# Performance work log

Hardware: AMD Instinct MI355X
Metric: run time of the kernel (lower is better)

Reference implementation:

```python
import jax, jax.numpy as jnp
import numpy as np

G, NP, C, H, L = 64, 512, 128, 4, 4
N = G * NP            # 32768 nodes
E = N * 16            # 524288 edges
HD = C // H
BN_EPS = 1e-5


def _bn(x, g, b):
    # BatchNorm1d, training-mode (biased batch statistics over nodes)
    m = x.mean(axis=0)
    v = jnp.var(x, axis=0)
    return (x - m) * jax.lax.rsqrt(v + BN_EPS) * g + b


def setup_inputs() -> dict:
    key = jax.random.key(0)
    ks = iter(jax.random.split(key, 64))
    rn = lambda shape, s=0.05: jax.random.normal(next(ks), shape, jnp.float32) * s
    inp = {}
    inp["x"] = jax.random.normal(next(ks), (N, 32), jnp.float32)
    inp["edge_attr"] = jax.random.normal(next(ks), (E, 16), jnp.float32)
    epg = E // G  # edges per graph; endpoints stay within each graph
    off = jnp.repeat(jnp.arange(G), epg) * NP
    src = jax.random.randint(next(ks), (E,), 0, NP) + off
    dst = jax.random.randint(next(ks), (E,), 0, NP) + off
    inp["edge_index"] = jnp.stack([src, dst]).astype(jnp.int32)
    inp["batch"] = jnp.repeat(jnp.arange(G), NP).astype(jnp.int32)
    inp["np_w"] = rn((32, C)); inp["np_b"] = jnp.zeros((C,), jnp.float32)
    inp["ep_w"] = rn((16, C)); inp["ep_b"] = jnp.zeros((C,), jnp.float32)
    inp["eps"] = jnp.zeros((L,), jnp.float32)  # GINEConv train_eps, init 0
    inp["gine_w1"] = rn((L, C, 2 * C)); inp["gine_b1"] = jnp.zeros((L, 2 * C), jnp.float32)
    inp["gine_w2"] = rn((L, 2 * C, C)); inp["gine_b2"] = jnp.zeros((L, C), jnp.float32)
    inp["attn_in_w"] = rn((L, 3 * C, C)); inp["attn_in_b"] = jnp.zeros((L, 3 * C), jnp.float32)
    inp["attn_out_w"] = rn((L, C, C)); inp["attn_out_b"] = jnp.zeros((L, C), jnp.float32)
    ones = jnp.ones((L, C), jnp.float32); zeros = jnp.zeros((L, C), jnp.float32)
    inp["bn1_g"], inp["bn1_b"] = ones, zeros
    inp["bn2_g"], inp["bn2_b"] = ones, zeros
    inp["bn3_g"], inp["bn3_b"] = ones, zeros
    inp["mlp_w1"] = rn((L, C, 2 * C)); inp["mlp_b1"] = jnp.zeros((L, 2 * C), jnp.float32)
    inp["mlp_w2"] = rn((L, 2 * C, C)); inp["mlp_b2"] = jnp.zeros((L, C), jnp.float32)
    inp["ln_g"] = jnp.ones((2 * C,), jnp.float32); inp["ln_b"] = jnp.zeros((2 * C,), jnp.float32)
    inp["head_w1"] = rn((2 * C, C)); inp["head_b1"] = jnp.zeros((C,), jnp.float32)
    inp["head_w2"] = rn((C, 1)); inp["head_b2"] = jnp.zeros((1,), jnp.float32)
    return inp


def reference(x, edge_attr, np_w, np_b, ep_w, ep_b, eps,
              gine_w1, gine_b1, gine_w2, gine_b2,
              attn_in_w, attn_in_b, attn_out_w, attn_out_b,
              bn1_g, bn1_b, bn2_g, bn2_b, bn3_g, bn3_b,
              mlp_w1, mlp_b1, mlp_w2, mlp_b2,
              ln_g, ln_b, head_w1, head_b1, head_w2, head_b2,
              edge_index, batch):
    h = x @ np_w + np_b                       # [N, C]
    e = edge_attr @ ep_w + ep_b               # [E, C]
    src, dst = edge_index[0], edge_index[1]   # PyG: row=source j, col=target i
    scale = 1.0 / np.sqrt(HD).astype(np.float32)
    for l in range(L):
        # ---- local GINEConv: relu(x_j + e) scatter-sum -> GELU MLP ----
        msg = jax.nn.relu(h[src] + e)                                 # [E, C]
        aggr = jax.ops.segment_sum(msg, dst, num_segments=N)          # [N, C]
        z = (1.0 + eps[l]) * h + aggr
        z = jax.nn.gelu(z @ gine_w1[l] + gine_b1[l], approximate=False) @ gine_w2[l] + gine_b2[l]
        h_local = _bn(z + h, bn1_g[l], bn1_b[l])
        # ---- global multihead attention on dense per-graph batch ----
        xd = h.reshape(G, NP, C)
        qkv = xd @ attn_in_w[l].T + attn_in_b[l]                      # [G, NP, 3C]
        q, k, v = jnp.split(qkv, 3, axis=-1)
        split_heads = lambda t: t.reshape(G, NP, H, HD).transpose(0, 2, 1, 3)
        q, k, v = split_heads(q), split_heads(k), split_heads(v)
        att = jax.nn.softmax(jnp.einsum('ghqd,ghkd->ghqk', q, k) * scale, axis=-1)
        o = jnp.einsum('ghqk,ghkd->ghqd', att, v).transpose(0, 2, 1, 3).reshape(N, C)
        o = o @ attn_out_w[l].T + attn_out_b[l]
        h_attn = _bn(o + h, bn2_g[l], bn2_b[l])
        # ---- combine + FFN ----
        out = h_local + h_attn
        m = jax.nn.relu(out @ mlp_w1[l] + mlp_b1[l]) @ mlp_w2[l] + mlp_b2[l]
        h = _bn(out + m, bn3_g[l], bn3_b[l])
    # ---- mean || max pooling over graphs ----
    cnt = jax.ops.segment_sum(jnp.ones((N, 1), h.dtype), batch, num_segments=G)
    x_mean = jax.ops.segment_sum(h, batch, num_segments=G) / cnt
    x_max = jax.ops.segment_max(h, batch, num_segments=G)
    g = jnp.concatenate([x_mean, x_max], axis=-1)                     # [G, 2C]
    mu = g.mean(-1, keepdims=True)
    var = jnp.var(g, axis=-1, keepdims=True)
    g = (g - mu) * jax.lax.rsqrt(var + 1e-5) * ln_g + ln_b
    g = jax.nn.gelu(g @ head_w1 + head_b1, approximate=False) @ head_w2 + head_b2
    return g.squeeze(-1)                                              # [G]
```

## Files before the change

### kernel.cpp

```cpp
#include <hip/hip_runtime.h>
#include <math.h>

typedef _Float16 f16;
typedef _Float16 f16x2 __attribute__((ext_vector_type(2)));
typedef _Float16 f16x4 __attribute__((ext_vector_type(4)));
typedef _Float16 f16x8 __attribute__((ext_vector_type(8)));
typedef float f32x4 __attribute__((ext_vector_type(4)));

#define G_ 64
#define NP_ 512
#define N_ 32768
#define E_ 524288
#define C_ 128
#define H_ 4
#define HD_ 32
#define L_ 4

static __device__ __forceinline__ float gelu_exact(float x) {
    return 0.5f * x * (1.0f + erff(x * 0.70710678118654752f));
}

__global__ __launch_bounds__(256) void k_prep(
    const float* __restrict__ g1, const float* __restrict__ g2,
    const float* __restrict__ m1, const float* __restrict__ m2,
    const float* __restrict__ ai, const float* __restrict__ ao,
    f16* __restrict__ g1t, f16* __restrict__ g2t,
    f16* __restrict__ m1t, f16* __restrict__ m2t,
    f16* __restrict__ ait, f16* __restrict__ aot)
{
    int i = blockIdx.x * 256 + threadIdx.x;
    if (i < 131072) {
        int l = i >> 15, r = i & 32767;
        int k = r >> 8, m = r & 255;
        g1t[l * 32768 + m * 128 + k] = (f16)g1[i];
    } else if (i < 262144) {
        int j = i - 131072;
        int l = j >> 15, r = j & 32767;
        int k = r >> 7, m = r & 127;
        g2t[l * 32768 + m * 256 + k] = (f16)g2[j];
    } else if (i < 393216) {
        int j = i - 262144;
        int l = j >> 15, r = j & 32767;
        int k = r >> 8, m = r & 255;
        m1t[l * 32768 + m * 128 + k] = (f16)m1[j];
    } else if (i < 524288) {
        int j = i - 393216;
        int l = j >> 15, r = j & 32767;
        int k = r >> 7, m = r & 127;
        m2t[l * 32768 + m * 256 + k] = (f16)m2[j];
    } else if (i < 720896) {
        int j = i - 524288;
        ait[j] = (f16)ai[j];
    } else if (i < 786432) {
        int j = i - 720896;
        aot[j] = (f16)ao[j];
    }
}

__global__ __launch_bounds__(256) void k_h0(const float* __restrict__ x,
    const float* __restrict__ w, const float* __restrict__ b,
    f16* __restrict__ h16)
{
    const int tid = threadIdx.x;
    const int lane = tid & 63, wid = tid >> 6;
    const int node = blockIdx.x * 4 + wid;
    const int c2 = lane * 2;
    float a0 = b[c2], a1 = b[c2 + 1];
    const float* xr = x + (size_t)node * 32;
#pragma unroll
    for (int k = 0; k < 32; k++) {
        float xv = xr[k];
        a0 += xv * w[k * 128 + c2];
        a1 += xv * w[k * 128 + c2 + 1];
    }
    f16x2 z; z[0] = (f16)a0; z[1] = (f16)a1;
    *(f16x2*)(h16 + (size_t)node * 128 + c2) = z;
}

__global__ void k_zero2(int* a, int* b) {
    int i = blockIdx.x * 256 + threadIdx.x;
    a[i] = 0; b[i] = 0;
}
__global__ void k_count(const int* __restrict__ ei, int* __restrict__ counts) {
    int e = blockIdx.x * 256 + threadIdx.x;
    atomicAdd(&counts[ei[E_ + e]], 1);
}
__global__ __launch_bounds__(1024) void k_scan(const int* __restrict__ counts,
                                               int* __restrict__ rowp)
{
    __shared__ int part[1024];
    const int t = threadIdx.x;
    int s = 0;
#pragma unroll
    for (int i = 0; i < 32; i++) s += counts[t * 32 + i];
    part[t] = s;
    __syncthreads();
    for (int off = 1; off < 1024; off <<= 1) {
        int u = (t >= off) ? part[t - off] : 0;
        __syncthreads();
        part[t] += u;
        __syncthreads();
    }
    int run = part[t] - s;
    for (int i = 0; i < 32; i++) {
        int c = counts[t * 32 + i];
        rowp[t * 32 + i] = run;
        run += c;
    }
    if (t == 1023) rowp[N_] = part[1023];
}
__global__ void k_fill(const int* __restrict__ ei, const int* __restrict__ rowp,
                       int* __restrict__ cursor, int* __restrict__ srcp,
                       int* __restrict__ eidp)
{
    int e = blockIdx.x * 256 + threadIdx.x;
    int d = ei[E_ + e];
    int p = atomicAdd(&cursor[d], 1);
    int pos = rowp[d] + p;
    srcp[pos] = ei[e];
    eidp[pos] = e;
}

__global__ __launch_bounds__(256) void k_edge(const float* __restrict__ edge_attr,
    const float* __restrict__ epw, const float* __restrict__ epb,
    const int* __restrict__ eidp, f16* __restrict__ e16p)
{
    __shared__ __align__(16) float rows[4][64][16];
    const int tid = threadIdx.x;
    const int lane = tid & 63, wid = tid >> 6;
    const int c2 = lane * 2;
    float w0[16], w1[16];
#pragma unroll
    for (int k = 0; k < 16; k++) {
        w0[k] = epw[k * 128 + c2];
        w1[k] = epw[k * 128 + c2 + 1];
    }
    const float b0 = epb[c2], b1 = epb[c2 + 1];
    const int gidx = blockIdx.x & 63, chunk = blockIdx.x >> 6;
    const int base = (gidx * 32 + chunk) * 256 + wid * 64;
    const int eidv = eidp[base + lane];
    const int er = lane >> 2, ec = lane & 3;
#pragma unroll
    for (int u = 0; u < 4; u++) {
        int e = __shfl(eidv, u * 16 + er);
        float4 v = *(const float4*)(edge_attr + (size_t)e * 16 + ec * 4);
        *(float4*)(&rows[wid][u * 16 + er][ec * 4]) = v;
    }
    for (int i = 0; i < 64; i++) {
        const float* r = &rows[wid][i][0];
        float4 q0 = *(const float4*)(r);
        float4 q1 = *(const float4*)(r + 4);
        float4 q2 = *(const float4*)(r + 8);
        float4 q3 = *(const float4*)(r + 12);
        float e0 = b0, e1 = b1;
        e0 += q0.x*w0[0] + q0.y*w0[1] + q0.z*w0[2] + q0.w*w0[3]
            + q1.x*w0[4] + q1.y*w0[5] + q1.z*w0[6] + q1.w*w0[7]
            + q2.x*w0[8] + q2.y*w0[9] + q2.z*w0[10] + q2.w*w0[11]
            + q3.x*w0[12] + q3.y*w0[13] + q3.z*w0[14] + q3.w*w0[15];
        e1 += q0.x*w1[0] + q0.y*w1[1] + q0.z*w1[2] + q0.w*w1[3]
            + q1.x*w1[4] + q1.y*w1[5] + q1.z*w1[6] + q1.w*w1[7]
            + q2.x*w1[8] + q2.y*w1[9] + q2.z*w1[10] + q2.w*w1[11]
            + q3.x*w1[12] + q3.y*w1[13] + q3.z*w1[14] + q3.w*w1[15];
        f16x2 z; z[0] = (f16)e0; z[1] = (f16)e1;
        *(f16x2*)(e16p + (size_t)(base + i) * 128 + c2) = z;
    }
}

__global__ __launch_bounds__(256) void k_aggr(const f16* __restrict__ h16,
    const f16* __restrict__ e16p, const int* __restrict__ srcp,
    const int* __restrict__ rowp, const float* __restrict__ eps, int layer,
    f16* __restrict__ zin)
{
    const int tid = threadIdx.x;
    const int lane = tid & 63, wid = tid >> 6;
    const int node = (blockIdx.x & 63) * 512 + (blockIdx.x >> 6) * 4 + wid;
    const int c2 = lane * 2;
    const int r0 = rowp[node], r1 = rowp[node + 1];
    const int deg = r1 - r0;
    const f16x2 hn = *(const f16x2*)(h16 + (size_t)node * 128 + c2);
    float a0 = 0.f, a1 = 0.f;
    if (deg > 0) {
        const int dd = deg < 64 ? deg : 64;
        const int jm = dd - 1;
        const int srcv = srcp[r0 + (lane < jm ? lane : jm)];
        f16x2 h_c, e_c, h_n, e_n;
        {
            int s = __shfl(srcv, 0);
            h_c = *(const f16x2*)(h16 + (size_t)s * 128 + c2);
            e_c = *(const f16x2*)(e16p + (size_t)r0 * 128 + c2);
            int j1 = 1 < jm ? 1 : jm;
            int s1 = __shfl(srcv, j1);
            h_n = *(const f16x2*)(h16 + (size_t)s1 * 128 + c2);
            e_n = *(const f16x2*)(e16p + (size_t)(r0 + j1) * 128 + c2);
        }
        for (int j = 0; j < dd; ++j) {
            int j2 = j + 2 < jm ? j + 2 : jm;
            int s2 = __shfl(srcv, j2);
            f16x2 h_f = *(const f16x2*)(h16 + (size_t)s2 * 128 + c2);
            f16x2 e_f = *(const f16x2*)(e16p + (size_t)(r0 + j2) * 128 + c2);
            a0 += fmaxf((float)e_c[0] + (float)h_c[0], 0.0f);
            a1 += fmaxf((float)e_c[1] + (float)h_c[1], 0.0f);
            h_c = h_n; e_c = e_n; h_n = h_f; e_n = e_f;
        }
        for (int pos = r0 + 64; pos < r1; ++pos) {
            int s = srcp[pos];
            f16x2 ev = *(const f16x2*)(e16p + (size_t)pos * 128 + c2);
            f16x2 hv = *(const f16x2*)(h16 + (size_t)s * 128 + c2);
            a0 += fmaxf((float)ev[0] + (float)hv[0], 0.0f);
            a1 += fmaxf((float)ev[1] + (float)hv[1], 0.0f);
        }
    }
    const float ep = 1.0f + eps[layer];
    f16x2 z;
    z[0] = (f16)(ep * (float)hn[0] + a0);
    z[1] = (f16)(ep * (float)hn[1] + a1);
    *(f16x2*)(zin + (size_t)node * 128 + c2) = z;
}

template <int KD, int EPI, bool COMB>
__global__ __launch_bounds__(256) void k_gemm(
    const f16* __restrict__ A, const f16* __restrict__ Bt,
    const float* __restrict__ bias,
    const f16* __restrict__ r1, const f16* __restrict__ r2,
    const float* __restrict__ sc1, const float* __restrict__ sc2,
    f16* __restrict__ out, f16* __restrict__ aout,
    float* __restrict__ stats, int Mout)
{
    __shared__ __align__(16) f16 As[64 * 40];
    __shared__ __align__(16) f16 Bs[128 * 40];
    __shared__ float sca[4][128];
    __shared__ float sscr[4][2][64];
    const int tid = threadIdx.x;
    const int lane = tid & 63, wid = tid >> 6;
    const int quad = lane >> 4, l16 = lane & 15;
    const int wm = wid >> 1, wn = wid & 1;
    const int rb = blockIdx.x, cb = blockIdx.y;
    if constexpr (COMB) {
        if (tid < 128) { sca[0][tid] = sc1[tid]; sca[1][tid] = sc1[128 + tid]; }
        else { int c = tid - 128; sca[2][c] = sc2[c]; sca[3][c] = sc2[128 + c]; }
    }
    f32x4 acc[2][4];
#pragma unroll
    for (int i = 0; i < 2; i++)
#pragma unroll
        for (int j = 0; j < 4; j++) acc[i][j] = {0.f, 0.f, 0.f, 0.f};
    const int arow0 = rb * 64, brow0 = cb * 128;
    const int srow = tid >> 2, sc4 = tid & 3;
#pragma unroll
    for (int kc = 0; kc < KD / 32; ++kc) {
        __syncthreads();
        if constexpr (COMB) {
            size_t off = (size_t)(arow0 + srow) * KD + kc * 32 + sc4 * 8;
            f16x8 x1 = *(const f16x8*)(r1 + off);
            f16x8 x2 = *(const f16x8*)(r2 + off);
            const int k0 = kc * 32 + sc4 * 8;
            f16x8 zc;
#pragma unroll
            for (int i = 0; i < 8; i++) {
                int k = k0 + i;
                float v = (float)x1[i] * sca[0][k] + sca[1][k]
                        + (float)x2[i] * sca[2][k] + sca[3][k];
                zc[i] = (f16)v;
            }
            *(f16x8*)(As + srow * 40 + sc4 * 8) = zc;
            if (cb == 0) *(f16x8*)(aout + off) = zc;
        } else {
            *(uint4*)(As + srow * 40 + sc4 * 8) =
                *(const uint4*)(A + (size_t)(arow0 + srow) * KD + kc * 32 + sc4 * 8);
        }
#pragma unroll
        for (int i = 0; i < 2; i++) {
            int j = tid + i * 256;
            int br = j >> 2, bc = j & 3;
            *(uint4*)(Bs + br * 40 + bc * 8) =
                *(const uint4*)(Bt + (size_t)(brow0 + br) * KD + kc * 32 + bc * 8);
        }
        __syncthreads();
        f16x8 af[2], bf[4];
#pragma unroll
        for (int mt = 0; mt < 2; mt++)
            af[mt] = *(const f16x8*)(As + (wm * 32 + mt * 16 + l16) * 40 + quad * 8);
#pragma unroll
        for (int nt = 0; nt < 4; nt++)
            bf[nt] = *(const f16x8*)(Bs + (wn * 64 + nt * 16 + l16) * 40 + quad * 8);
#pragma unroll
        for (int mt = 0; mt < 2; mt++)
#pragma unroll
            for (int nt = 0; nt < 4; nt++)
                acc[mt][nt] = __builtin_amdgcn_mfma_f32_16x16x32_f16(
                    af[mt], bf[nt], acc[mt][nt], 0, 0, 0);
    }
    float ssum[4] = {0, 0, 0, 0}, ssq[4] = {0, 0, 0, 0};
#pragma unroll
    for (int nt = 0; nt < 4; nt++) {
        const int col = cb * 128 + wn * 64 + nt * 16 + l16;
        const float bv = bias[col];
#pragma unroll
        for (int mt = 0; mt < 2; mt++) {
#pragma unroll
            for (int r = 0; r < 4; r++) {
                const int row = rb * 64 + wm * 32 + mt * 16 + quad * 4 + r;
                float v = acc[mt][nt][r] + bv;
                if constexpr (EPI == 0) v = gelu_exact(v);
                if constexpr (EPI == 1) v = fmaxf(v, 0.0f);
                if constexpr (EPI == 2) {
                    v += (float)r1[(size_t)row * 128 + col];
                    ssum[nt] += v;
                    ssq[nt] += v * v;
                }
                out[(size_t)row * Mout + col] = (f16)v;
            }
        }
    }
    if constexpr (EPI == 2) {
#pragma unroll
        for (int nt = 0; nt < 4; nt++) {
            float s = ssum[nt], q = ssq[nt];
            s += __shfl_xor(s, 16); s += __shfl_xor(s, 32);
            q += __shfl_xor(q, 16); q += __shfl_xor(q, 32);
            if (lane < 16) {
                sscr[wid][0][nt * 16 + lane] = s;
                sscr[wid][1][nt * 16 + lane] = q;
            }
        }
        __syncthreads();
        if (tid < 128) {
            int c = tid, wnc = c >> 6, jj = c & 63;
            stats[(size_t)rb * 256 + c] = sscr[wnc][0][jj] + sscr[wnc + 2][0][jj];
            stats[(size_t)rb * 256 + 128 + c] = sscr[wnc][1][jj] + sscr[wnc + 2][1][jj];
        }
    }
}

__global__ __launch_bounds__(256) void k_qkv(
    const f16* __restrict__ A, const f16* __restrict__ Bt,
    const float* __restrict__ bias,
    f16* __restrict__ qb, f16* __restrict__ kb, f16* __restrict__ vt)
{
    __shared__ __align__(16) f16 As[64 * 40];
    __shared__ __align__(16) f16 Bs[128 * 40];
    const int tid = threadIdx.x;
    const int lane = tid & 63, wid = tid >> 6;
    const int quad = lane >> 4, l16 = lane & 15;
    const int wm = wid >> 1, wn = wid & 1;
    const int rb = blockIdx.x, cb = blockIdx.y;
    f32x4 acc[2][4];
#pragma unroll
    for (int i = 0; i < 2; i++)
#pragma unroll
        for (int j = 0; j < 4; j++) acc[i][j] = {0.f, 0.f, 0.f, 0.f};
    const int arow0 = rb * 64, brow0 = cb * 128;
    const int srow = tid >> 2, sc4 = tid & 3;
#pragma unroll
    for (int kc = 0; kc < 4; ++kc) {
        __syncthreads();
        *(uint4*)(As + srow * 40 + sc4 * 8) =
            *(const uint4*)(A + (size_t)(arow0 + srow) * 128 + kc * 32 + sc4 * 8);
#pragma unroll
        for (int i = 0; i < 2; i++) {
            int j = tid + i * 256;
            int br = j >> 2, bc = j & 3;
            *(uint4*)(Bs + br * 40 + bc * 8) =
                *(const uint4*)(Bt + (size_t)(brow0 + br) * 128 + kc * 32 + bc * 8);
        }
        __syncthreads();
        f16x8 af[2], bf[4];
#pragma unroll
        for (int mt = 0; mt < 2; mt++)
            af[mt] = *(const f16x8*)(As + (wm * 32 + mt * 16 + l16) * 40 + quad * 8);
#pragma unroll
        for (int nt = 0; nt < 4; nt++)
            bf[nt] = *(const f16x8*)(Bs + (wn * 64 + nt * 16 + l16) * 40 + quad * 8);
#pragma unroll
        for (int mt = 0; mt < 2; mt++)
#pragma unroll
            for (int nt = 0; nt < 4; nt++)
                acc[mt][nt] = __builtin_amdgcn_mfma_f32_16x16x32_f16(
                    af[mt], bf[nt], acc[mt][nt], 0, 0, 0);
    }
    if (cb < 2) {
        f16* outp = cb ? kb : qb;
#pragma unroll
        for (int nt = 0; nt < 4; nt++) {
            const int col = wn * 64 + nt * 16 + l16;
            const float bv = bias[cb * 128 + col];
#pragma unroll
            for (int mt = 0; mt < 2; mt++) {
#pragma unroll
                for (int r = 0; r < 4; r++) {
                    const int row = rb * 64 + wm * 32 + mt * 16 + quad * 4 + r;
                    outp[(size_t)row * 128 + col] = (f16)(acc[mt][nt][r] + bv);
                }
            }
        }
    } else {
        const int g = rb >> 3;
#pragma unroll
        for (int nt = 0; nt < 4; nt++) {
            const int coll = wn * 64 + nt * 16 + l16;
            const int h = coll >> 5, d = coll & 31;
            const float bv = bias[256 + coll];
#pragma unroll
            for (int mt = 0; mt < 2; mt++) {
                const int n0 = (rb & 7) * 64 + wm * 32 + mt * 16 + quad * 4;
                f16x4 z;
#pragma unroll
                for (int r = 0; r < 4; r++) z[r] = (f16)(acc[mt][nt][r] + bv);
                *(f16x4*)(vt + ((size_t)((g * 4 + h) * 32 + d)) * 512 + n0) = z;
            }
        }
    }
}

__global__ __launch_bounds__(1024) void k_fin(
    const float* __restrict__ sA, const float* __restrict__ sB,
    const float* __restrict__ g1, const float* __restrict__ b1,
    const float* __restrict__ g2, const float* __restrict__ b2,
    float* __restrict__ o1, float* __restrict__ o2)
{
    __shared__ float rS[8][128], rQ[8][128];
    const float* s = blockIdx.x ? sB : sA;
    const float* g = blockIdx.x ? g2 : g1;
    const float* bb = blockIdx.x ? b2 : b1;
    float* o = blockIdx.x ? o2 : o1;
    const int c = threadIdx.x & 127, seg = threadIdx.x >> 7;
    float S = 0, Q = 0;
    for (int b = seg * 64; b < seg * 64 + 64; b++) {
        S += s[b * 256 + c];
        Q += s[b * 256 + 128 + c];
    }
    rS[seg][c] = S; rQ[seg][c] = Q;
    __syncthreads();
    if (threadIdx.x < 128) {
        float Ss = 0, Qs = 0;
#pragma unroll
        for (int k = 0; k < 8; k++) { Ss += rS[k][c]; Qs += rQ[k][c]; }
        float mean = Ss * (1.0f / 32768.0f);
        float var = Qs * (1.0f / 32768.0f) - mean * mean;
        float rstd = rsqrtf(var + 1e-5f);
        float scv = g[c] * rstd;
        o[c] = scv;
        o[128 + c] = bb[c] - mean * scv;
    }
}

__global__ __launch_bounds__(256) void k_bn3(const f16* __restrict__ t3,
    const float* __restrict__ s3, f16* __restrict__ h16)
{
    int i = blockIdx.x * 256 + threadIdx.x;
    int n = i >> 6, c2 = (i & 63) * 2;
    f16x2 a = *(const f16x2*)(t3 + (size_t)n * 128 + c2);
    f16x2 z;
    z[0] = (f16)((float)a[0] * s3[c2] + s3[128 + c2]);
    z[1] = (f16)((float)a[1] * s3[c2 + 1] + s3[129 + c2]);
    *(f16x2*)(h16 + (size_t)n * 128 + c2) = z;
}

__global__ __launch_bounds__(256) void k_attn(const f16* __restrict__ qb,
    const f16* __restrict__ kb, const f16* __restrict__ vt, f16* __restrict__ o)
{
    __shared__ __align__(16) f16 Ks[512 * 40];
    __shared__ __align__(16) f16 Ps[4][16 * 40];
    const int tid = threadIdx.x;
    const int lane = tid & 63, wid = tid >> 6;
    const int quad = lane >> 4, l16 = lane & 15;
    const int blk = blockIdx.x;
    const int gh = blk & 255, qc = blk >> 8;
    const int g = gh >> 2, h = gh & 3;
#pragma unroll
    for (int i = 0; i < 8; i++) {
        int j = i * 256 + tid;
        int n = j >> 2, c4 = j & 3;
        *(uint4*)(Ks + n * 40 + c4 * 8) =
            *(const uint4*)(kb + (size_t)(g * 512 + n) * 128 + h * 32 + c4 * 8);
    }
    const int node = g * 512 + qc * 64 + wid * 16 + l16;
    f16x8 aq = *(const f16x8*)(qb + (size_t)node * 128 + h * 32 + quad * 8);
    __syncthreads();
    const f32x4 zero = {0.f, 0.f, 0.f, 0.f};
    const float cexp = 0.17677669529663689f * 1.44269504088896341f;
    float mx = -1e30f;
    for (int kt = 0; kt < 32; ++kt) {
        f16x8 ak = *(const f16x8*)(Ks + (kt * 16 + l16) * 40 + quad * 8);
        f32x4 s = __builtin_amdgcn_mfma_f32_16x16x32_f16(ak, aq, zero, 0, 0, 0);
        mx = fmaxf(mx, fmaxf(fmaxf(s[0], s[1]), fmaxf(s[2], s[3])));
    }
    mx = fmaxf(mx, __shfl_xor(mx, 16));
    mx = fmaxf(mx, __shfl_xor(mx, 32));
    float lsum = 0.f;
    f32x4 o0 = {0.f, 0.f, 0.f, 0.f}, o1 = {0.f, 0.f, 0.f, 0.f};
    f16* pp = &Ps[wid][0];
    const f16* vbase = vt + (size_t)gh * 32 * 512;
    for (int ch = 0; ch < 16; ++ch) {
#pragma unroll
        for (int hf = 0; hf < 2; ++hf) {
            int kt = ch * 2 + hf;
            f16x8 ak = *(const f16x8*)(Ks + (kt * 16 + l16) * 40 + quad * 8);
            f32x4 s = __builtin_amdgcn_mfma_f32_16x16x32_f16(ak, aq, zero, 0, 0, 0);
            f16x4 pk;
#pragma unroll
            for (int r = 0; r < 4; r++) {
                float p = exp2f((s[r] - mx) * cexp);
                lsum += p;
                pk[r] = (f16)p;
            }
            *(f16x4*)(pp + l16 * 40 + hf * 16 + quad * 4) = pk;
        }
        f16x8 ap = *(const f16x8*)(pp + l16 * 40 + quad * 8);
        f16x8 bv0 = *(const f16x8*)(vbase + (size_t)l16 * 512 + ch * 32 + quad * 8);
        f16x8 bv1 = *(const f16x8*)(vbase + (size_t)(16 + l16) * 512 + ch * 32 + quad * 8);
        o0 = __builtin_amdgcn_mfma_f32_16x16x32_f16(ap, bv0, o0, 0, 0, 0);
        o1 = __builtin_amdgcn_mfma_f32_16x16x32_f16(ap, bv1, o1, 0, 0, 0);
    }
    lsum += __shfl_xor(lsum, 16);
    lsum += __shfl_xor(lsum, 32);
    const float linv = 1.0f / lsum;
#pragma unroll
    for (int r = 0; r < 4; r++) {
        float li = __shfl(linv, quad * 4 + r);
        int nrow = g * 512 + qc * 64 + wid * 16 + quad * 4 + r;
        o[(size_t)nrow * 128 + h * 32 + l16] = (f16)(o0[r] * li);
        o[(size_t)nrow * 128 + h * 32 + 16 + l16] = (f16)(o1[r] * li);
    }
}

__global__ __launch_bounds__(256) void k_pool(const f16* __restrict__ h16,
    const float* __restrict__ ln_g, const float* __restrict__ ln_b,
    const float* __restrict__ w1, const float* __restrict__ b1,
    const float* __restrict__ w2, const float* __restrict__ b2,
    float* __restrict__ outp)
{
    __shared__ float ssum[4][128], smax[4][128];
    __shared__ float gl[256];
    __shared__ float red[256];
    __shared__ float hid[128];
    __shared__ float stat[2];
    const int tid = threadIdx.x, lane = tid & 63, wid = tid >> 6;
    const int g = blockIdx.x;
    const int c2 = lane * 2;
    float s0 = 0, s1 = 0, m0 = -1e30f, m1 = -1e30f;
    for (int i = 0; i < 128; i++) {
        int n = g * 512 + i * 4 + wid;
        f16x2 hv = *(const f16x2*)(h16 + (size_t)n * 128 + c2);
        float v0 = (float)hv[0], v1 = (float)hv[1];
        s0 += v0; s1 += v1;
        m0 = fmaxf(m0, v0); m1 = fmaxf(m1, v1);
    }
    ssum[wid][c2] = s0; ssum[wid][c2 + 1] = s1;
    smax[wid][c2] = m0; smax[wid][c2 + 1] = m1;
    __syncthreads();
    if (tid < 128) {
        float S = ssum[0][tid] + ssum[1][tid] + ssum[2][tid] + ssum[3][tid];
        float M = fmaxf(fmaxf(smax[0][tid], smax[1][tid]),
                        fmaxf(smax[2][tid], smax[3][tid]));
        gl[tid] = S * (1.0f / 512.0f);
        gl[128 + tid] = M;
    }
    __syncthreads();
    float v = gl[tid];
    red[tid] = v;
    __syncthreads();
    for (int off = 128; off > 0; off >>= 1) {
        if (tid < off) red[tid] += red[tid + off];
        __syncthreads();
    }
    if (tid == 0) stat[0] = red[0] * (1.0f / 256.0f);
    __syncthreads();
    float mu = stat[0];
    red[tid] = (v - mu) * (v - mu);
    __syncthreads();
    for (int off = 128; off > 0; off >>= 1) {
        if (tid < off) red[tid] += red[tid + off];
        __syncthreads();
    }
    if (tid == 0) stat[1] = rsqrtf(red[0] * (1.0f / 256.0f) + 1e-5f);
    __syncthreads();
    float gn = (v - mu) * stat[1] * ln_g[tid] + ln_b[tid];
    __syncthreads();
    gl[tid] = gn;
    __syncthreads();
    if (tid < 128) {
        float a = b1[tid];
        for (int k = 0; k < 256; k++) a += gl[k] * w1[k * 128 + tid];
        hid[tid] = gelu_exact(a);
    }
    __syncthreads();
    if (tid < 64) {
        float a = hid[tid] * w2[tid] + hid[tid + 64] * w2[tid + 64];
        a += __shfl_xor(a, 32); a += __shfl_xor(a, 16); a += __shfl_xor(a, 8);
        a += __shfl_xor(a, 4); a += __shfl_xor(a, 2); a += __shfl_xor(a, 1);
        if (tid == 0) outp[g] = a + b2[0];
    }
}

extern "C" void kernel_launch(void* const* d_in, const int* in_sizes, int n_in,
                              void* d_out, int out_size, void* d_ws, size_t ws_size,
                              hipStream_t stream)
{
    const float* x          = (const float*)d_in[0];
    const float* edge_attr  = (const float*)d_in[1];
    const int*   ei         = (const int*)d_in[2];
    const float* np_w       = (const float*)d_in[4];
    const float* np_b       = (const float*)d_in[5];
    const float* ep_w       = (const float*)d_in[6];
    const float* ep_b       = (const float*)d_in[7];
    const float* eps        = (const float*)d_in[8];
    const float* gine_w1    = (const float*)d_in[9];
    const float* gine_b1    = (const float*)d_in[10];
    const float* gine_w2    = (const float*)d_in[11];
    const float* gine_b2    = (const float*)d_in[12];
    const float* attn_in_w  = (const float*)d_in[13];
    const float* attn_in_b  = (const float*)d_in[14];
    const float* attn_out_w = (const float*)d_in[15];
    const float* attn_out_b = (const float*)d_in[16];
    const float* bn1_g      = (const float*)d_in[17];
    const float* bn1_b      = (const float*)d_in[18];
    const float* bn2_g      = (const float*)d_in[19];
    const float* bn2_b      = (const float*)d_in[20];
    const float* bn3_g      = (const float*)d_in[21];
    const float* bn3_b      = (const float*)d_in[22];
    const float* mlp_w1     = (const float*)d_in[23];
    const float* mlp_b1     = (const float*)d_in[24];
    const float* mlp_w2     = (const float*)d_in[25];
    const float* mlp_b2     = (const float*)d_in[26];
    const float* ln_g       = (const float*)d_in[27];
    const float* ln_b       = (const float*)d_in[28];
    const float* head_w1    = (const float*)d_in[29];
    const float* head_b1    = (const float*)d_in[30];
    const float* head_w2    = (const float*)d_in[31];
    const float* head_b2    = (const float*)d_in[32];

    char* ws = (char*)d_ws;
    size_t off = 0;
    auto alloc = [&](size_t bytes) {
        void* p = ws + off;
        off += (bytes + 255) & ~(size_t)255;
        return p;
    };
    f16*  h16    = (f16*)alloc((size_t)N_ * 128 * 2);
    f16*  zin    = (f16*)alloc((size_t)N_ * 128 * 2);
    f16*  tloc   = (f16*)alloc((size_t)N_ * 128 * 2);
    f16*  tattn  = (f16*)alloc((size_t)N_ * 128 * 2);
    f16*  out16  = (f16*)alloc((size_t)N_ * 128 * 2);
    f16*  o16    = (f16*)alloc((size_t)N_ * 128 * 2);
    f16*  u16    = (f16*)alloc((size_t)N_ * 256 * 2);
    float* statsA = (float*)alloc(512 * 256 * 4);
    float* statsB = (float*)alloc(512 * 256 * 4);
    float* scsh1  = (float*)alloc(256 * 4);
    float* scsh2  = (float*)alloc(256 * 4);
    float* scsh3  = (float*)alloc(256 * 4);
    int*  rowp   = (int*)alloc((N_ + 1) * 4);
    int*  counts = (int*)alloc(N_ * 4);
    int*  cursor = (int*)alloc(N_ * 4);
    int*  srcp   = (int*)alloc((size_t)E_ * 4);
    int*  eidp   = (int*)alloc((size_t)E_ * 4);
    f16*  g1t    = (f16*)alloc((size_t)L_ * 32768 * 2);
    f16*  g2t    = (f16*)alloc((size_t)L_ * 32768 * 2);
    f16*  m1t    = (f16*)alloc((size_t)L_ * 32768 * 2);
    f16*  m2t    = (f16*)alloc((size_t)L_ * 32768 * 2);
    f16*  ait    = (f16*)alloc((size_t)L_ * 49152 * 2);
    f16*  aot    = (f16*)alloc((size_t)L_ * 16384 * 2);
    f16*  e16p   = (f16*)alloc((size_t)E_ * 128 * 2);
    f16*  qbuf = zin;
    f16*  kbuf = out16;
    f16*  vt   = u16 + (size_t)N_ * 128;

    dim3 B(256);
    k_prep<<<dim3(3072), B, 0, stream>>>(gine_w1, gine_w2, mlp_w1, mlp_w2,
                                         attn_in_w, attn_out_w,
                                         g1t, g2t, m1t, m2t, ait, aot);
    k_h0<<<dim3(8192), B, 0, stream>>>(x, np_w, np_b, h16);
    k_zero2<<<dim3(128), B, 0, stream>>>(counts, cursor);
    k_count<<<dim3(2048), B, 0, stream>>>(ei, counts);
    k_scan<<<dim3(1), dim3(1024), 0, stream>>>(counts, rowp);
    k_fill<<<dim3(2048), B, 0, stream>>>(ei, rowp, cursor, srcp, eidp);
    k_edge<<<dim3(2048), B, 0, stream>>>(edge_attr, ep_w, ep_b, eidp, e16p);

    const f16* nf = (const f16*)nullptr;
    const float* nff = (const float*)nullptr;
    for (int l = 0; l < L_; l++) {
        k_aggr<<<dim3(8192), B, 0, stream>>>(h16, e16p, srcp, rowp, eps, l, zin);
        k_gemm<128, 0, false><<<dim3(512, 2), B, 0, stream>>>(
            zin, g1t + l * 32768, gine_b1 + l * 256, nf, nf, nff, nff,
            u16, (f16*)nullptr, (float*)nullptr, 256);
        k_gemm<256, 2, false><<<dim3(512, 1), B, 0, stream>>>(
            u16, g2t + l * 32768, gine_b2 + l * 128, h16, nf, nff, nff,
            tloc, (f16*)nullptr, statsA, 128);
        k_qkv<<<dim3(512, 3), B, 0, stream>>>(
            h16, ait + l * 49152, attn_in_b + l * 384, qbuf, kbuf, vt);
        k_attn<<<dim3(2048), B, 0, stream>>>(qbuf, kbuf, vt, o16);
        k_gemm<128, 2, false><<<dim3(512, 1), B, 0, stream>>>(
            o16, aot + l * 16384, attn_out_b + l * 128, h16, nf, nff, nff,
            tattn, (f16*)nullptr, statsB, 128);
        k_fin<<<dim3(2), dim3(1024), 0, stream>>>(
            statsA, statsB, bn1_g + l * 128, bn1_b + l * 128,
            bn2_g + l * 128, bn2_b + l * 128, scsh1, scsh2);
        k_gemm<128, 1, true><<<dim3(512, 2), B, 0, stream>>>(
            nf, m1t + l * 32768, mlp_b1 + l * 256, tloc, tattn, scsh1, scsh2,
            u16, out16, (float*)nullptr, 256);
        k_gemm<256, 2, false><<<dim3(512, 1), B, 0, stream>>>(
            u16, m2t + l * 32768, mlp_b2 + l * 128, out16, nf, nff, nff,
            zin, (f16*)nullptr, statsA, 128);
        k_fin<<<dim3(1), dim3(1024), 0, stream>>>(
            statsA, statsA, bn3_g + l * 128, bn3_b + l * 128,
            bn3_g + l * 128, bn3_b + l * 128, scsh3, scsh3);
        k_bn3<<<dim3(8192), B, 0, stream>>>(zin, scsh3, h16);
    }
    k_pool<<<dim3(64), B, 0, stream>>>(h16, ln_g, ln_b, head_w1, head_b1,
                                       head_w2, head_b2, (float*)d_out);
}
```

Baseline: 1.003 ms.

## Load GEMM fragments directly from global, split combine kernel, make attention online-softmax

```diff
diff --git a/kernel.cpp b/kernel.cpp
--- a/kernel.cpp
+++ b/kernel.cpp
@@ -217,94 +217,57 @@
     *(f16x2*)(zin + (size_t)node * 128 + c2) = z;
 }
 
-template <int KD, int EPI, bool COMB>
+template <int KD, int EPI>
 __global__ __launch_bounds__(256) void k_gemm(
     const f16* __restrict__ A, const f16* __restrict__ Bt,
-    const float* __restrict__ bias,
-    const f16* __restrict__ r1, const f16* __restrict__ r2,
-    const float* __restrict__ sc1, const float* __restrict__ sc2,
-    f16* __restrict__ out, f16* __restrict__ aout,
-    float* __restrict__ stats, int Mout)
-{
-    __shared__ __align__(16) f16 As[64 * 40];
-    __shared__ __align__(16) f16 Bs[128 * 40];
-    __shared__ float sca[4][128];
+    const float* __restrict__ bias, const f16* __restrict__ resid,
+    f16* __restrict__ out, float* __restrict__ stats, int Mout)
+{
     __shared__ float sscr[4][2][64];
     const int tid = threadIdx.x;
     const int lane = tid & 63, wid = tid >> 6;
     const int quad = lane >> 4, l16 = lane & 15;
     const int wm = wid >> 1, wn = wid & 1;
     const int rb = blockIdx.x, cb = blockIdx.y;
-    if constexpr (COMB) {
-        if (tid < 128) { sca[0][tid] = sc1[tid]; sca[1][tid] = sc1[128 + tid]; }
-        else { int c = tid - 128; sca[2][c] = sc2[c]; sca[3][c] = sc2[128 + c]; }
-    }
+    const int row0 = rb * 64 + wm * 32;
+    const int col0 = cb * 128 + wn * 64;
     f32x4 acc[2][4];
 #pragma unroll
     for (int i = 0; i < 2; i++)
 #pragma unroll
         for (int j = 0; j < 4; j++) acc[i][j] = {0.f, 0.f, 0.f, 0.f};
-    const int arow0 = rb * 64, brow0 = cb * 128;
-    const int srow = tid >> 2, sc4 = tid & 3;
+    const f16* ap0 = A + (size_t)(row0 + l16) * KD + quad * 8;
+    const f16* ap1 = ap0 + (size_t)16 * KD;
+    const f16* bp  = Bt + (size_t)(col0 + l16) * KD + quad * 8;
 #pragma unroll
     for (int kc = 0; kc < KD / 32; ++kc) {
-        __syncthreads();
-        if constexpr (COMB) {
-            size_t off = (size_t)(arow0 + srow) * KD + kc * 32 + sc4 * 8;
-            f16x8 x1 = *(const f16x8*)(r1 + off);
-            f16x8 x2 = *(const f16x8*)(r2 + off);
-            const int k0 = kc * 32 + sc4 * 8;
-            f16x8 zc;
-#pragma unroll
-            for (int i = 0; i < 8; i++) {
-                int k = k0 + i;
-                float v = (float)x1[i] * sca[0][k] + sca[1][k]
-                        + (float)x2[i] * sca[2][k] + sca[3][k];
-                zc[i] = (f16)v;
-            }
-            *(f16x8*)(As + srow * 40 + sc4 * 8) = zc;
-            if (cb == 0) *(f16x8*)(aout + off) = zc;
-        } else {
-            *(uint4*)(As + srow * 40 + sc4 * 8) =
-                *(const uint4*)(A + (size_t)(arow0 + srow) * KD + kc * 32 + sc4 * 8);
-        }
-#pragma unroll
-        for (int i = 0; i < 2; i++) {
-            int j = tid + i * 256;
-            int br = j >> 2, bc = j & 3;
-            *(uint4*)(Bs + br * 40 + bc * 8) =
-                *(const uint4*)(Bt + (size_t)(brow0 + br) * KD + kc * 32 + bc * 8);
-        }
-        __syncthreads();
-        f16x8 af[2], bf[4];
-#pragma unroll
-        for (int mt = 0; mt < 2; mt++)
-            af[mt] = *(const f16x8*)(As + (wm * 32 + mt * 16 + l16) * 40 + quad * 8);
+        f16x8 af0 = *(const f16x8*)(ap0 + kc * 32);
+        f16x8 af1 = *(const f16x8*)(ap1 + kc * 32);
+        f16x8 bf[4];
 #pragma unroll
         for (int nt = 0; nt < 4; nt++)
-            bf[nt] = *(const f16x8*)(Bs + (wn * 64 + nt * 16 + l16) * 40 + quad * 8);
-#pragma unroll
-        for (int mt = 0; mt < 2; mt++)
-#pragma unroll
-            for (int nt = 0; nt < 4; nt++)
-                acc[mt][nt] = __builtin_amdgcn_mfma_f32_16x16x32_f16(
-                    af[mt], bf[nt], acc[mt][nt], 0, 0, 0);
+            bf[nt] = *(const f16x8*)(bp + (size_t)nt * 16 * KD + kc * 32);
+#pragma unroll
+        for (int nt = 0; nt < 4; nt++) {
+            acc[0][nt] = __builtin_amdgcn_mfma_f32_16x16x32_f16(af0, bf[nt], acc[0][nt], 0, 0, 0);
+            acc[1][nt] = __builtin_amdgcn_mfma_f32_16x16x32_f16(af1, bf[nt], acc[1][nt], 0, 0, 0);
+        }
     }
     float ssum[4] = {0, 0, 0, 0}, ssq[4] = {0, 0, 0, 0};
 #pragma unroll
     for (int nt = 0; nt < 4; nt++) {
-        const int col = cb * 128 + wn * 64 + nt * 16 + l16;
+        const int col = col0 + nt * 16 + l16;
         const float bv = bias[col];
 #pragma unroll
         for (int mt = 0; mt < 2; mt++) {
 #pragma unroll
             for (int r = 0; r < 4; r++) {
-                const int row = rb * 64 + wm * 32 + mt * 16 + quad * 4 + r;
+                const int row = row0 + mt * 16 + quad * 4 + r;
                 float v = acc[mt][nt][r] + bv;
                 if constexpr (EPI == 0) v = gelu_exact(v);
                 if constexpr (EPI == 1) v = fmaxf(v, 0.0f);
                 if constexpr (EPI == 2) {
-                    v += (float)r1[(size_t)row * 128 + col];
+                    v += (float)resid[(size_t)row * 128 + col];
                     ssum[nt] += v;
                     ssq[nt] += v * v;
                 }
@@ -337,46 +300,33 @@
     const float* __restrict__ bias,
     f16* __restrict__ qb, f16* __restrict__ kb, f16* __restrict__ vt)
 {
-    __shared__ __align__(16) f16 As[64 * 40];
-    __shared__ __align__(16) f16 Bs[128 * 40];
     const int tid = threadIdx.x;
     const int lane = tid & 63, wid = tid >> 6;
     const int quad = lane >> 4, l16 = lane & 15;
     const int wm = wid >> 1, wn = wid & 1;
     const int rb = blockIdx.x, cb = blockIdx.y;
+    const int row0 = rb * 64 + wm * 32;
     f32x4 acc[2][4];
 #pragma unroll
     for (int i = 0; i < 2; i++)
 #pragma unroll
         for (int j = 0; j < 4; j++) acc[i][j] = {0.f, 0.f, 0.f, 0.f};
-    const int arow0 = rb * 64, brow0 = cb * 128;
-    const int srow = tid >> 2, sc4 = tid & 3;
+    const f16* ap0 = A + (size_t)(row0 + l16) * 128 + quad * 8;
+    const f16* ap1 = ap0 + 16 * 128;
+    const f16* bp  = Bt + (size_t)(cb * 128 + wn * 64 + l16) * 128 + quad * 8;
 #pragma unroll
     for (int kc = 0; kc < 4; ++kc) {
-        __syncthreads();
-        *(uint4*)(As + srow * 40 + sc4 * 8) =
-            *(const uint4*)(A + (size_t)(arow0 + srow) * 128 + kc * 32 + sc4 * 8);
-#pragma unroll
-        for (int i = 0; i < 2; i++) {
-            int j = tid + i * 256;
-            int br = j >> 2, bc = j & 3;
-            *(uint4*)(Bs + br * 40 + bc * 8) =
-                *(const uint4*)(Bt + (size_t)(brow0 + br) * 128 + kc * 32 + bc * 8);
-        }
-        __syncthreads();
-        f16x8 af[2], bf[4];
-#pragma unroll
-        for (int mt = 0; mt < 2; mt++)
-            af[mt] = *(const f16x8*)(As + (wm * 32 + mt * 16 + l16) * 40 + quad * 8);
+        f16x8 af0 = *(const f16x8*)(ap0 + kc * 32);
+        f16x8 af1 = *(const f16x8*)(ap1 + kc * 32);
+        f16x8 bf[4];
 #pragma unroll
         for (int nt = 0; nt < 4; nt++)
-            bf[nt] = *(const f16x8*)(Bs + (wn * 64 + nt * 16 + l16) * 40 + quad * 8);
-#pragma unroll
-        for (int mt = 0; mt < 2; mt++)
-#pragma unroll
-            for (int nt = 0; nt < 4; nt++)
-                acc[mt][nt] = __builtin_amdgcn_mfma_f32_16x16x32_f16(
-                    af[mt], bf[nt], acc[mt][nt], 0, 0, 0);
+            bf[nt] = *(const f16x8*)(bp + (size_t)nt * 16 * 128 + kc * 32);
+#pragma unroll
+        for (int nt = 0; nt < 4; nt++) {
+            acc[0][nt] = __builtin_amdgcn_mfma_f32_16x16x32_f16(af0, bf[nt], acc[0][nt], 0, 0, 0);
+            acc[1][nt] = __builtin_amdgcn_mfma_f32_16x16x32_f16(af1, bf[nt], acc[1][nt], 0, 0, 0);
+        }
     }
     if (cb < 2) {
         f16* outp = cb ? kb : qb;
@@ -388,7 +338,7 @@
             for (int mt = 0; mt < 2; mt++) {
 #pragma unroll
                 for (int r = 0; r < 4; r++) {
-                    const int row = rb * 64 + wm * 32 + mt * 16 + quad * 4 + r;
+                    const int row = row0 + mt * 16 + quad * 4 + r;
                     outp[(size_t)row * 128 + col] = (f16)(acc[mt][nt][r] + bv);
                 }
             }
@@ -444,6 +394,20 @@
     }
 }
 
+__global__ __launch_bounds__(256) void k_combine(const f16* __restrict__ tloc,
+    const f16* __restrict__ tattn, const float* __restrict__ s1,
+    const float* __restrict__ s2, f16* __restrict__ out)
+{
+    int i = blockIdx.x * 256 + threadIdx.x;
+    int n = i >> 6, c2 = (i & 63) * 2;
+    f16x2 a = *(const f16x2*)(tloc + (size_t)n * 128 + c2);
+    f16x2 b = *(const f16x2*)(tattn + (size_t)n * 128 + c2);
+    f16x2 z;
+    z[0] = (f16)((float)a[0] * s1[c2] + s1[128 + c2] + (float)b[0] * s2[c2] + s2[128 + c2]);
+    z[1] = (f16)((float)a[1] * s1[c2 + 1] + s1[129 + c2] + (float)b[1] * s2[c2 + 1] + s2[129 + c2]);
+    *(f16x2*)(out + (size_t)n * 128 + c2) = z;
+}
+
 __global__ __launch_bounds__(256) void k_bn3(const f16* __restrict__ t3,
     const float* __restrict__ s3, f16* __restrict__ h16)
 {
@@ -459,8 +423,8 @@
 __global__ __launch_bounds__(256) void k_attn(const f16* __restrict__ qb,
     const f16* __restrict__ kb, const f16* __restrict__ vt, f16* __restrict__ o)
 {
-    __shared__ __align__(16) f16 Ks[512 * 40];
-    __shared__ __align__(16) f16 Ps[4][16 * 40];
+    __shared__ __align__(16) f16 Ks[512 * 36];
+    __shared__ __align__(16) f16 Ps[4][512];
     const int tid = threadIdx.x;
     const int lane = tid & 63, wid = tid >> 6;
     const int quad = lane >> 4, l16 = lane & 15;
@@ -471,7 +435,7 @@
     for (int i = 0; i < 8; i++) {
         int j = i * 256 + tid;
         int n = j >> 2, c4 = j & 3;
-        *(uint4*)(Ks + n * 40 + c4 * 8) =
+        *(uint4*)(Ks + n * 36 + c4 * 8) =
             *(const uint4*)(kb + (size_t)(g * 512 + n) * 128 + h * 32 + c4 * 8);
     }
     const int node = g * 512 + qc * 64 + wid * 16 + l16;
@@ -479,34 +443,45 @@
     __syncthreads();
     const f32x4 zero = {0.f, 0.f, 0.f, 0.f};
     const float cexp = 0.17677669529663689f * 1.44269504088896341f;
-    float mx = -1e30f;
-    for (int kt = 0; kt < 32; ++kt) {
-        f16x8 ak = *(const f16x8*)(Ks + (kt * 16 + l16) * 40 + quad * 8);
-        f32x4 s = __builtin_amdgcn_mfma_f32_16x16x32_f16(ak, aq, zero, 0, 0, 0);
-        mx = fmaxf(mx, fmaxf(fmaxf(s[0], s[1]), fmaxf(s[2], s[3])));
-    }
-    mx = fmaxf(mx, __shfl_xor(mx, 16));
-    mx = fmaxf(mx, __shfl_xor(mx, 32));
-    float lsum = 0.f;
+    float m = -1e30f, lsum = 0.f;
     f32x4 o0 = {0.f, 0.f, 0.f, 0.f}, o1 = {0.f, 0.f, 0.f, 0.f};
     f16* pp = &Ps[wid][0];
     const f16* vbase = vt + (size_t)gh * 32 * 512;
+    const int roff = ((quad & 2) ? 256 : 0) + ((quad & 1) ? 128 : 0);
     for (int ch = 0; ch < 16; ++ch) {
-#pragma unroll
-        for (int hf = 0; hf < 2; ++hf) {
-            int kt = ch * 2 + hf;
-            f16x8 ak = *(const f16x8*)(Ks + (kt * 16 + l16) * 40 + quad * 8);
-            f32x4 s = __builtin_amdgcn_mfma_f32_16x16x32_f16(ak, aq, zero, 0, 0, 0);
-            f16x4 pk;
-#pragma unroll
-            for (int r = 0; r < 4; r++) {
-                float p = exp2f((s[r] - mx) * cexp);
-                lsum += p;
-                pk[r] = (f16)p;
-            }
-            *(f16x4*)(pp + l16 * 40 + hf * 16 + quad * 4) = pk;
-        }
-        f16x8 ap = *(const f16x8*)(pp + l16 * 40 + quad * 8);
+        f16x8 ak0 = *(const f16x8*)(Ks + ((2 * ch) * 16 + l16) * 36 + quad * 8);
+        f16x8 ak1 = *(const f16x8*)(Ks + ((2 * ch + 1) * 16 + l16) * 36 + quad * 8);
+        f32x4 s0 = __builtin_amdgcn_mfma_f32_16x16x32_f16(ak0, aq, zero, 0, 0, 0);
+        f32x4 s1 = __builtin_amdgcn_mfma_f32_16x16x32_f16(ak1, aq, zero, 0, 0, 0);
+        float cm = fmaxf(fmaxf(fmaxf(s0[0], s0[1]), fmaxf(s0[2], s0[3])),
+                         fmaxf(fmaxf(s1[0], s1[1]), fmaxf(s1[2], s1[3])));
+        cm = fmaxf(cm, __shfl_xor(cm, 16));
+        cm = fmaxf(cm, __shfl_xor(cm, 32));
+        float mn = fmaxf(m, cm);
+        float alpha = exp2f((m - mn) * cexp);
+        m = mn;
+        f16x4 p0, p1;
+        float ps = 0.f;
+#pragma unroll
+        for (int r = 0; r < 4; r++) {
+            float e0 = exp2f((s0[r] - m) * cexp);
+            float e1 = exp2f((s1[r] - m) * cexp);
+            ps += e0 + e1;
+            p0[r] = (f16)e0; p1[r] = (f16)e1;
+        }
+        lsum = lsum * alpha + ps;
+        *(f16x4*)(pp + lane * 4) = p0;
+        *(f16x4*)(pp + 256 + lane * 4) = p1;
+#pragma unroll
+        for (int r = 0; r < 4; r++) {
+            float ar = __shfl(alpha, quad * 4 + r);
+            o0[r] *= ar; o1[r] *= ar;
+        }
+        f16x4 a_lo = *(const f16x4*)(pp + roff + l16 * 4);
+        f16x4 a_hi = *(const f16x4*)(pp + roff + 64 + l16 * 4);
+        f16x8 ap;
+#pragma unroll
+        for (int i2 = 0; i2 < 4; i2++) { ap[i2] = a_lo[i2]; ap[i2 + 4] = a_hi[i2]; }
         f16x8 bv0 = *(const f16x8*)(vbase + (size_t)l16 * 512 + ch * 32 + quad * 8);
         f16x8 bv1 = *(const f16x8*)(vbase + (size_t)(16 + l16) * 512 + ch * 32 + quad * 8);
         o0 = __builtin_amdgcn_mfma_f32_16x16x32_f16(ap, bv0, o0, 0, 0, 0);
@@ -677,30 +652,30 @@
     k_edge<<<dim3(2048), B, 0, stream>>>(edge_attr, ep_w, ep_b, eidp, e16p);
 
     const f16* nf = (const f16*)nullptr;
-    const float* nff = (const float*)nullptr;
     for (int l = 0; l < L_; l++) {
         k_aggr<<<dim3(8192), B, 0, stream>>>(h16, e16p, srcp, rowp, eps, l, zin);
-        k_gemm<128, 0, false><<<dim3(512, 2), B, 0, stream>>>(
-            zin, g1t + l * 32768, gine_b1 + l * 256, nf, nf, nff, nff,
-            u16, (f16*)nullptr, (float*)nullptr, 256);
-        k_gemm<256, 2, false><<<dim3(512, 1), B, 0, stream>>>(
-            u16, g2t + l * 32768, gine_b2 + l * 128, h16, nf, nff, nff,
-            tloc, (f16*)nullptr, statsA, 128);
+        k_gemm<128, 0><<<dim3(512, 2), B, 0, stream>>>(
+            zin, g1t + l * 32768, gine_b1 + l * 256, nf,
+            u16, (float*)nullptr, 256);
+        k_gemm<256, 2><<<dim3(512, 1), B, 0, stream>>>(
+            u16, g2t + l * 32768, gine_b2 + l * 128, h16,
+            tloc, statsA, 128);
         k_qkv<<<dim3(512, 3), B, 0, stream>>>(
             h16, ait + l * 49152, attn_in_b + l * 384, qbuf, kbuf, vt);
         k_attn<<<dim3(2048), B, 0, stream>>>(qbuf, kbuf, vt, o16);
-        k_gemm<128, 2, false><<<dim3(512, 1), B, 0, stream>>>(
-            o16, aot + l * 16384, attn_out_b + l * 128, h16, nf, nff, nff,
-            tattn, (f16*)nullptr, statsB, 128);
+        k_gemm<128, 2><<<dim3(512, 1), B, 0, stream>>>(
+            o16, aot + l * 16384, attn_out_b + l * 128, h16,
+            tattn, statsB, 128);
         k_fin<<<dim3(2), dim3(1024), 0, stream>>>(
             statsA, statsB, bn1_g + l * 128, bn1_b + l * 128,
             bn2_g + l * 128, bn2_b + l * 128, scsh1, scsh2);
-        k_gemm<128, 1, true><<<dim3(512, 2), B, 0, stream>>>(
-            nf, m1t + l * 32768, mlp_b1 + l * 256, tloc, tattn, scsh1, scsh2,
-            u16, out16, (float*)nullptr, 256);
-        k_gemm<256, 2, false><<<dim3(512, 1), B, 0, stream>>>(
-            u16, m2t + l * 32768, mlp_b2 + l * 128, out16, nf, nff, nff,
-            zin, (f16*)nullptr, statsA, 128);
+        k_combine<<<dim3(8192), B, 0, stream>>>(tloc, tattn, scsh1, scsh2, out16);
+        k_gemm<128, 1><<<dim3(512, 2), B, 0, stream>>>(
+            out16, m1t + l * 32768, mlp_b1 + l * 256, nf,
+            u16, (float*)nullptr, 256);
+        k_gemm<256, 2><<<dim3(512, 1), B, 0, stream>>>(
+            u16, m2t + l * 32768, mlp_b2 + l * 128, out16,
+            zin, statsA, 128);
         k_fin<<<dim3(1), dim3(1024), 0, stream>>>(
             statsA, statsA, bn3_g + l * 128, bn3_b + l * 128,
             bn3_g + l * 128, bn3_b + l * 128, scsh3, scsh3);
```

After: 1.129 ms. 12.6% more time.
